# Optimization experiments

Measured on AMD Instinct MI355X. Metric: run time of the kernel, lower is better.

The kernel has to match this reference:

```python
import jax, jax.numpy as jnp
import numpy as np
import math

B, S, D, NH = 2, 2048, 1024, 16
DK = D // NH
E, TOPK, MOE_H, NSH = 8, 2, 1024, 2
SH_H = MOE_H * NSH
EPS = 1e-6


def setup_inputs() -> dict:
    key = jax.random.key(0)
    ks = jax.random.split(key, 24)
    p = lambda k, shape: jax.random.normal(k, shape, jnp.float32) * 0.02
    x = jax.random.normal(ks[0], (B, S, D), jnp.float32)
    # RoPE tables: freqs_cis = exp(i * t * theta^{-2j/dk}), passed as cos/sin
    inv = 1.0 / (10000.0 ** (np.arange(0, DK, 2, dtype=np.float32) / DK))
    ang = np.outer(np.arange(S, dtype=np.float32), inv)
    freqs_cos = jnp.asarray(np.cos(ang), jnp.float32)
    freqs_sin = jnp.asarray(np.sin(ang), jnp.float32)
    mask = jnp.triu(jnp.full((S, S), -1e9, jnp.float32), k=1)  # causal additive mask
    return {
        'x': x, 'freqs_cos': freqs_cos, 'freqs_sin': freqs_sin, 'mask': mask,
        'wq': p(ks[1], (D, D)), 'wk': p(ks[2], (D, D)),
        'wv': p(ks[3], (D, D)), 'wo': p(ks[4], (D, D)),
        'attn_norm_w': jnp.ones((D,), jnp.float32),
        'ffn_norm_w': jnp.ones((D,), jnp.float32),
        'gate_w': p(ks[5], (E, D)), 'gate_b': p(ks[6], (E,)),
        'w1': p(ks[7], (E, MOE_H, D)), 'b1': p(ks[8], (E, MOE_H)),
        'w2': p(ks[9], (E, D, MOE_H)), 'b2': p(ks[10], (E, D)),
        'w3': p(ks[11], (E, MOE_H, D)), 'b3': p(ks[12], (E, MOE_H)),
        'sg_w': p(ks[13], (SH_H, D)), 'su_w': p(ks[14], (SH_H, D)),
        'sd_w': p(ks[15], (D, SH_H)),
    }


def rmsnorm(x, w):
    f = x.astype(jnp.float32)
    y = f * jax.lax.rsqrt(jnp.mean(f * f, axis=-1, keepdims=True) + EPS)
    return y.astype(x.dtype) * w


def rope(t, cos, sin):
    # t: [b, s, h, dk]; pairs (t[2j], t[2j+1]) as complex, multiplied by e^{i ang}
    tr, ti = t[..., 0::2], t[..., 1::2]
    c, s = cos[None, :, None, :], sin[None, :, None, :]
    outr = tr * c - ti * s
    outi = tr * s + ti * c
    return jnp.stack([outr, outi], axis=-1).reshape(t.shape)


def reference(x, freqs_cos, freqs_sin, mask, wq, wk, wv, wo, attn_norm_w, ffn_norm_w,
              gate_w, gate_b, w1, b1, w2, b2, w3, b3, sg_w, su_w, sd_w):
    b, s, d = x.shape
    # --- attention with RoPE ---
    h = rmsnorm(x, attn_norm_w)
    q = (h @ wq.T).reshape(b, s, NH, DK)
    k = (h @ wk.T).reshape(b, s, NH, DK)
    v = (h @ wv.T).reshape(b, s, NH, DK)
    q = rope(q, freqs_cos, freqs_sin)
    k = rope(k, freqs_cos, freqs_sin)
    scale = 1.0 / math.sqrt(DK)
    q = q.transpose(0, 2, 1, 3)
    k = k.transpose(0, 2, 1, 3)
    v = v.transpose(0, 2, 1, 3)
    scores = jnp.einsum('bhqd,bhkd->bhqk', q, k) * scale + mask
    # NOTE: source divides by sqrt(d_k) a second time before softmax (faithful quirk)
    attn = jax.nn.softmax(scores * scale, axis=-1)
    o = jnp.einsum('bhqk,bhkd->bhqd', attn, v).transpose(0, 2, 1, 3).reshape(b, s, d)
    x = x + o @ wo.T
    # --- MoE FFN ---
    hf = rmsnorm(x, ffn_norm_w).reshape(-1, d)                 # [T, D]
    gscores = jax.nn.softmax(hf @ gate_w.T + gate_b, axis=-1)  # [T, E]
    _, idx = jax.lax.top_k(gscores, TOPK)                      # bias is None -> topk on scores
    weights = jnp.take_along_axis(gscores, idx, axis=1)        # original_scores gather
    wmask = (jax.nn.one_hot(idx, E, dtype=hf.dtype) * weights[..., None]).sum(1)  # [T, E]
    shared = (jax.nn.silu(hf @ sg_w.T) * (hf @ su_w.T)) @ sd_w.T
    a1 = jnp.einsum('td,ehd->teh', hf, w1) + b1
    a3 = jnp.einsum('td,ehd->teh', hf, w3) + b3
    eo = jnp.einsum('teh,edh->ted', jax.nn.silu(a1) * a3, w2) + b2  # [T, E, D]
    router = jnp.einsum('te,ted->td', wmask, eo)
    return x + (shared + router).reshape(x.shape)
```

## Files before the change

kernel.cpp:

```cpp
#include <hip/hip_runtime.h>


typedef unsigned short u16;
typedef __attribute__((ext_vector_type(8))) short bh8;
typedef __attribute__((ext_vector_type(4))) float fv4;
typedef __attribute__((ext_vector_type(4))) unsigned uv4;
typedef __attribute__((ext_vector_type(2))) int iv2;

#define LOG2E 1.4426950408889634f
#define MAX_TILES 71

__device__ __forceinline__ float b2f(u16 u) {
  return __builtin_bit_cast(float, ((unsigned)u) << 16);
}
__device__ __forceinline__ u16 f2b(float f) {
  unsigned x = __builtin_bit_cast(unsigned, f);
  return (u16)((x + 0x7fffu + ((x >> 16) & 1u)) >> 16);
}
__device__ __forceinline__ fv4 mfma16(bh8 a, bh8 b, fv4 c) {
  return __builtin_amdgcn_mfma_f32_16x16x32_bf16(a, b, c, 0, 0, 0);
}
__device__ __forceinline__ unsigned cvtpk(float lo, float hi) {
  unsigned r;
  asm("v_cvt_pk_bf16_f32 %0, %1, %2" : "=v"(r) : "v"(lo), "v"(hi));
  return r;
}

__device__ __forceinline__ int xcd_swizzle1d(int flat, int nwg) {
  int q = nwg >> 3, r = nwg & 7;
  int xcd = flat & 7, idx = flat >> 3;
  return (xcd < r ? xcd * (q + 1) : r * (q + 1) + (xcd - r) * q) + idx;
}

#define GLD16(g, l)                                                        \
  __builtin_amdgcn_global_load_lds(                                        \
      (const __attribute__((address_space(1))) void*)(g),                  \
      (__attribute__((address_space(3))) void*)(l), 16, 0, 0)

__device__ __forceinline__ bh8 lds_frag(const u16* base, int row, int b8) {
  int off = row * 128 + ((b8 * 16) ^ ((row & 7) << 4));
  return *(const bh8*)((const char*)base + off);
}

template <int MODE, int TM>
__device__ __forceinline__ void gemm_body(
    u16* AsB, u16* BsB, int bx, int by, const u16* __restrict__ A,
    const u16* __restrict__ B, int M, int N, int K, u16* __restrict__ Cb,
    float* __restrict__ Cf, const float* __restrict__ add1,
    const float* __restrict__ add2, const float* __restrict__ bias,
    const int* __restrict__ tmeta, const int* __restrict__ etok) {
  constexpr int MR = TM / 32;
  constexpr int ACL = TM / 64;
  const int lane = threadIdx.x & 63;
  const int wid = threadIdx.x >> 6;
  const int wr = wid >> 2, wc = wid & 3;
  const int n0 = bx * 128;
  const int l15 = lane & 15;
  const int rr = lane >> 3;
  const int b8s = (lane & 7) ^ rr;
  const int ldA = (MODE == 6) ? M : K;

  int m0 = 0, e = 0, m0l = 0, cnt = 0, row0 = 0;
  const u16* Bp = B;
  if constexpr (MODE == 6 || MODE == 8) {
    int tile = by, half = 0;
    if constexpr (MODE == 6 && TM == 64) {
      tile = by >> 1;
      half = by & 1;
    }
    if (tile >= tmeta[0]) return;
    e = tmeta[16 + tile * 4];
    m0l = tmeta[17 + tile * 4];
    cnt = tmeta[18 + tile * 4];
    row0 = tmeta[19 + tile * 4] + half * 64;
    Bp = B + (size_t)e * N * K;
  } else {
    m0 = by * TM;
  }

  const u16* Arow[ACL];
  const u16* Brow[2];
#pragma unroll
  for (int i = 0; i < ACL; ++i) {
    int c = wid * ACL + i;
    int row = c * 8 + rr;
    if constexpr (MODE == 8) {
      int li = m0l + row;
      li = li < cnt ? li : cnt - 1;
      int tok = etok[e * 4096 + li];
      Arow[i] = A + (size_t)tok * ldA + b8s * 8;
    } else if constexpr (MODE == 6) {
      Arow[i] = A + (size_t)(row0 + row) * ldA + b8s * 8;
    } else {
      Arow[i] = A + (size_t)(m0 + row) * ldA + b8s * 8;
    }
  }
#pragma unroll
  for (int i = 0; i < 2; ++i)
    Brow[i] = Bp + (size_t)(n0 + (wid * 2 + i) * 8 + rr) * K + b8s * 8;

  fv4 acc[MR][2] = {};
  const int nt = K >> 6;

#pragma unroll
  for (int i = 0; i < ACL; ++i)
    GLD16(Arow[i], &AsB[(wid * ACL + i) * 512]);
#pragma unroll
  for (int i = 0; i < 2; ++i)
    GLD16(Brow[i], &BsB[(wid * 2 + i) * 512]);

  for (int t = 0; t < nt; ++t) {
    const int cur = t & 1;
    u16* Asc = AsB + cur * (TM * 64);
    u16* Bsc = BsB + cur * (128 * 64);
    if (t + 1 < nt) {
      const int k0 = (t + 1) * 64;
      u16* Asn = AsB + (cur ^ 1) * (TM * 64);
      u16* Bsn = BsB + (cur ^ 1) * (128 * 64);
#pragma unroll
      for (int i = 0; i < ACL; ++i)
        GLD16(Arow[i] + k0, &Asn[(wid * ACL + i) * 512]);
#pragma unroll
      for (int i = 0; i < 2; ++i)
        GLD16(Brow[i] + k0, &Bsn[(wid * 2 + i) * 512]);
      if constexpr (ACL == 2)
        asm volatile("s_waitcnt vmcnt(4)" ::: "memory");
      else
        asm volatile("s_waitcnt vmcnt(3)" ::: "memory");
    } else {
      asm volatile("s_waitcnt vmcnt(0)" ::: "memory");
    }
    __builtin_amdgcn_s_barrier();
    __builtin_amdgcn_sched_barrier(0);

#pragma unroll
    for (int ks = 0; ks < 2; ++ks) {
      int b8 = ks * 4 + (lane >> 4);
      bh8 af[MR], bf[2];
#pragma unroll
      for (int mi = 0; mi < MR; ++mi)
        af[mi] = lds_frag(Asc, wr * (16 * MR) + mi * 16 + l15, b8);
      if constexpr (MODE == 7 || MODE == 8) {
        int col0 = (wc >> 1) * 64 + (wc & 1) * 16;
        bf[0] = lds_frag(Bsc, col0 + l15, b8);
        bf[1] = lds_frag(Bsc, col0 + 32 + l15, b8);
      } else {
#pragma unroll
        for (int ni = 0; ni < 2; ++ni)
          bf[ni] = lds_frag(Bsc, wc * 32 + ni * 16 + l15, b8);
      }
      __builtin_amdgcn_s_setprio(1);
#pragma unroll
      for (int mi = 0; mi < MR; ++mi)
#pragma unroll
        for (int ni = 0; ni < 2; ++ni)
          acc[mi][ni] = mfma16(af[mi], bf[ni], acc[mi][ni]);
      __builtin_amdgcn_s_setprio(0);
    }
    __builtin_amdgcn_sched_barrier(0);
    __builtin_amdgcn_s_barrier();
    __builtin_amdgcn_sched_barrier(0);
  }

  const int rbase = (MODE == 6 || MODE == 8) ? row0 : m0;
  const int r0b = rbase + wr * (16 * MR) + (lane >> 4) * 4;

  if constexpr (MODE == 7 || MODE == 8) {
    const int OUTN = N >> 1;
    const int c = (n0 >> 1) + (wc >> 1) * 32 + (wc & 1) * 16 + l15;
    const float* bb1 = nullptr;
    const float* bb3 = nullptr;
    if constexpr (MODE == 8) {
      bb1 = add1 + (size_t)e * OUTN;
      bb3 = add2 + (size_t)e * OUTN;
    }
#pragma unroll
    for (int mi = 0; mi < MR; ++mi) {
#pragma unroll
      for (int r = 0; r < 4; ++r) {
        int row = r0b + mi * 16 + r;
        float xg = acc[mi][0][r];
        float yu = acc[mi][1][r];
        if constexpr (MODE == 8) {
          xg += bb1[c];
          yu += bb3[c];
        }
        float s = xg / (1.f + __expf(-xg));
        Cb[(size_t)row * OUTN + c] = f2b(s * yu);
      }
    }
  } else if constexpr (MODE == 9) {
    const int c0b = n0 + wc * 32 + l15;
#pragma unroll
    for (int mi = 0; mi < MR; ++mi) {
#pragma unroll
      for (int r = 0; r < 4; ++r) {
        int row = r0b + mi * 16 + r;
        int g0 = tmeta[2 * row], g1 = tmeta[2 * row + 1];
        float w0 = bias[2 * row], w1 = bias[2 * row + 1];
        const u16* e0p = Cb + (size_t)g0 * 1024;
        const u16* e1p = Cb + (size_t)g1 * 1024;
#pragma unroll
        for (int ni = 0; ni < 2; ++ni) {
          int c = c0b + ni * 16;
          size_t idx = (size_t)row * N + c;
          Cf[idx] = add1[idx] + acc[mi][ni][r] + w0 * b2f(e0p[c]) +
                    w1 * b2f(e1p[c]);
        }
      }
    }
  } else {
    const int c0b = n0 + wc * 32 + l15;
    const float* bb = nullptr;
    if constexpr (MODE == 6) bb = bias + (size_t)e * N;
#pragma unroll
    for (int mi = 0; mi < MR; ++mi) {
#pragma unroll
      for (int ni = 0; ni < 2; ++ni) {
        int c = c0b + ni * 16;
#pragma unroll
        for (int r = 0; r < 4; ++r) {
          int row = r0b + mi * 16 + r;
          size_t idx = (size_t)row * N + c;
          float v = acc[mi][ni][r];
          if constexpr (MODE == 0) Cb[idx] = f2b(v);
          else if constexpr (MODE == 1) Cf[idx] = add1[idx] + v;
          else Cb[idx] = f2b(v + bb[c]);
        }
      }
    }
  }
}

template <int MODE, int TM = 128, int STILE = 0>
__global__ __launch_bounds__(512) void gemm_bt(
    const u16* __restrict__ A, const u16* __restrict__ B, int M, int N, int K,
    u16* __restrict__ Cb, float* __restrict__ Cf,
    const float* __restrict__ add1, const float* __restrict__ add2,
    const float* __restrict__ bias, const int* __restrict__ tmeta,
    const int* __restrict__ etok) {
  __shared__ u16 As[2][TM * 64];
  __shared__ u16 Bs[2][128 * 64];
  const int gx = gridDim.x;
  int flat = (int)blockIdx.y * gx + (int)blockIdx.x;
  flat = xcd_swizzle1d(flat, gx * (int)gridDim.y);
  int bx, by;
  if constexpr (STILE) {
    int SX = gx >> 2;
    int sidx = flat >> 5, within = flat & 31;
    int sy = sidx / SX, sx = sidx - sy * SX;
    by = sy * 8 + (within >> 2);
    bx = sx * 4 + (within & 3);
  } else {
    by = flat / gx;
    bx = flat - by * gx;
  }
  gemm_body<MODE, TM>(&As[0][0], &Bs[0][0], bx, by, A, B, M, N, K, Cb, Cf,
                      add1, add2, bias, tmeta, etok);
}

__global__ __launch_bounds__(512) void gemm_sgu_w13(
    const u16* __restrict__ hf, const u16* __restrict__ sgu_w,
    u16* __restrict__ hs, const u16* __restrict__ w13_w,
    u16* __restrict__ a13, const float* __restrict__ b1,
    const float* __restrict__ b3, const int* __restrict__ meta,
    const int* __restrict__ etok) {
  __shared__ u16 As[2][128 * 64];
  __shared__ u16 Bs[2][128 * 64];
  const int nwg = 1024 + 16 * MAX_TILES;
  int flat = xcd_swizzle1d((int)blockIdx.x, nwg);
  if (flat < 1024) {
    int sidx = flat >> 5, within = flat & 31;
    int sy = sidx >> 3, sx = sidx & 7;
    int by = sy * 8 + (within >> 2);
    int bx = sx * 4 + (within & 3);
    gemm_body<7, 128>(&As[0][0], &Bs[0][0], bx, by, hf, sgu_w, 4096, 4096,
                      1024, hs, nullptr, nullptr, nullptr, nullptr, nullptr,
                      nullptr);
  } else {
    int idx = flat - 1024;
    int by = idx >> 4, bx = idx & 15;
    gemm_body<8, 128>(&As[0][0], &Bs[0][0], bx, by, hf, w13_w, 4096, 2048,
                      1024, a13, nullptr, b1, b3, nullptr, meta, etok);
  }
}

__device__ __forceinline__ void conv_plain(const float* src, u16* dst,
                                           int lb) {
  size_t i = ((size_t)lb * 256 + threadIdx.x) * 8;
  fv4 a = *(const fv4*)(src + i);
  fv4 b = *(const fv4*)(src + i + 4);
  bh8 o;
#pragma unroll
  for (int j = 0; j < 4; ++j) o[j] = (short)f2b(a[j]);
#pragma unroll
  for (int j = 0; j < 4; ++j) o[4 + j] = (short)f2b(b[j]);
  *(bh8*)(dst + i) = o;
}
__device__ __forceinline__ void conv_ilv(const float* src, u16* dst, int lb,
                                         int half, int seg_shift) {
  size_t i = ((size_t)lb * 256 + threadIdx.x) * 8;
  int r = (int)(i >> 10), col = (int)(i & 1023);
  int rl = r & ((1 << seg_shift) - 1), e = r >> seg_shift;
  int dstrow = (e << (seg_shift + 1)) + ((rl >> 5) << 6) + (rl & 31) +
               (half << 5);
  fv4 a = *(const fv4*)(src + i);
  fv4 b = *(const fv4*)(src + i + 4);
  bh8 o;
#pragma unroll
  for (int j = 0; j < 4; ++j) o[j] = (short)f2b(a[j]);
#pragma unroll
  for (int j = 0; j < 4; ++j) o[4 + j] = (short)f2b(b[j]);
  *(bh8*)(dst + (size_t)dstrow * 1024 + col) = o;
}

__global__ __launch_bounds__(256) void mega_prep(
    const float* __restrict__ wq, const float* __restrict__ wk,
    const float* __restrict__ wv, const float* __restrict__ wo,
    const float* __restrict__ sdw, const float* __restrict__ w2,
    const float* __restrict__ sgw, const float* __restrict__ suw,
    const float* __restrict__ w1, const float* __restrict__ w3,
    const float* __restrict__ x, const float* __restrict__ anw,
    u16* __restrict__ wqkv_b, u16* __restrict__ wo_b,
    u16* __restrict__ sdw_b, u16* __restrict__ w2_b,
    u16* __restrict__ sgu_b, u16* __restrict__ w13_b,
    u16* __restrict__ h_b) {
  __shared__ float red[4];
  const int bid = blockIdx.x;
  if (bid < 512) {
    conv_plain(wq, wqkv_b, bid);
  } else if (bid < 1024) {
    conv_plain(wk, wqkv_b + 1048576, bid - 512);
  } else if (bid < 1536) {
    conv_plain(wv, wqkv_b + 2097152, bid - 1024);
  } else if (bid < 2048) {
    conv_plain(wo, wo_b, bid - 1536);
  } else if (bid < 3072) {
    conv_plain(sdw, sdw_b, bid - 2048);
  } else if (bid < 7168) {
    conv_plain(w2, w2_b, bid - 3072);
  } else if (bid < 8192) {
    conv_ilv(sgw, sgu_b, bid - 7168, 0, 11);
  } else if (bid < 9216) {
    conv_ilv(suw, sgu_b, bid - 8192, 1, 11);
  } else if (bid < 13312) {
    conv_ilv(w1, w13_b, bid - 9216, 0, 10);
  } else if (bid < 17408) {
    conv_ilv(w3, w13_b, bid - 13312, 1, 10);
  } else {
    int t = bid - 17408;
    const float* xr = x + (size_t)t * 1024;
    fv4 v = *(const fv4*)(xr + threadIdx.x * 4);
    float ss = v[0] * v[0] + v[1] * v[1] + v[2] * v[2] + v[3] * v[3];
#pragma unroll
    for (int off = 1; off < 64; off <<= 1) ss += __shfl_xor(ss, off);
    int lane = threadIdx.x & 63, wid = threadIdx.x >> 6;
    if (lane == 0) red[wid] = ss;
    __syncthreads();
    float inv =
        rsqrtf((red[0] + red[1] + red[2] + red[3]) * (1.0f / 1024.f) + 1e-6f);
    u16* op = h_b + (size_t)t * 1024 + threadIdx.x * 4;
    const float* wp = anw + threadIdx.x * 4;
#pragma unroll
    for (int i = 0; i < 4; ++i) op[i] = f2b(v[i] * inv * wp[i]);
  }
}

__global__ __launch_bounds__(256) void rope_repack(
    const u16* __restrict__ qkv, const float* __restrict__ fc,
    const float* __restrict__ fs, u16* __restrict__ qr, u16* __restrict__ kr,
    u16* __restrict__ vt, int S) {
  __shared__ u16 tile[64][65];
  const int s0 = blockIdx.x * 64;
  const int b = blockIdx.y;
  const int h0 = blockIdx.z * 4;
#pragma unroll 4
  for (int it = 0; it < 32; ++it) {
    int idx = threadIdx.x + it * 256;
    int tl = idx >> 7, rem = idx & 127;
    int h = h0 + (rem >> 5), i = rem & 31;
    int s = s0 + tl;
    float c = fc[s * 32 + i], sn = fs[s * 32 + i];
    size_t src = ((size_t)(b * S + s)) * 3072 + h * 64 + 2 * i;
    size_t dst = ((size_t)((b * 16 + h) * S + s)) * 64 + 2 * i;
    float a0 = b2f(qkv[src]), a1 = b2f(qkv[src + 1]);
    qr[dst] = f2b(a0 * c - a1 * sn);
    qr[dst + 1] = f2b(a0 * sn + a1 * c);
    float b0 = b2f(qkv[src + 1024]), b1 = b2f(qkv[src + 1025]);
    kr[dst] = f2b(b0 * c - b1 * sn);
    kr[dst + 1] = f2b(b0 * sn + b1 * c);
  }
  for (int hh = 0; hh < 4; ++hh) {
    int h = h0 + hh;
    __syncthreads();
    for (int cc = threadIdx.x; cc < 512; cc += 256) {
      int tl = cc >> 3, d8 = cc & 7;
      bh8 val = *(const bh8*)(qkv + ((size_t)(b * S + s0 + tl)) * 3072 + 2048 +
                              h * 64 + d8 * 8);
#pragma unroll
      for (int j = 0; j < 8; ++j) tile[tl][d8 * 8 + j] = (u16)val[j];
    }
    __syncthreads();
    for (int cc = threadIdx.x; cc < 512; cc += 256) {
      int d = cc >> 3, pg = cc & 7;
      int sbase = 16 * (pg >> 2) + 4 * (pg & 3);
      bh8 o;
#pragma unroll
      for (int j = 0; j < 8; ++j)
        o[j] = (short)tile[sbase + (j & 3) + ((j >> 2) << 5)][d];
      *(bh8*)(vt + ((size_t)((b * 16 + h) * 64 + d)) * S + s0 + pg * 8) = o;
    }
  }
}

__global__ __launch_bounds__(256) void attn_fwd(
    const u16* __restrict__ qr, const u16* __restrict__ kr,
    const u16* __restrict__ vt, u16* __restrict__ ob, int S, int NHc) {
  __shared__ u16 Ks[2][2][64 * 64];
  __shared__ u16 Vs[2][2][64 * 64];
  const int lane = threadIdx.x & 63;
  const int wid = threadIdx.x >> 6;
  const int g = lane >> 4;
  const int l15 = lane & 15;
  const int bh = blockIdx.x;
  const int ia = blockIdx.y;
  const int nq = S / 64;
  const int qa0 = ia * 64;
  const int qb0 = (nq - 1 - ia) * 64;
  const int b = bh / NHc, h = bh % NHc;
  const u16* qbase = qr + (size_t)bh * S * 64;
  const u16* kb = kr + (size_t)bh * S * 64;
  const u16* vb = vt + (size_t)bh * 64 * S;
  const float SC = 0.015625f * LOG2E;
  const int rr = lane >> 3;
  const int b8s = (lane & 7) ^ rr;

  bh8 ONES;
#pragma unroll
  for (int j = 0; j < 8; ++j) ONES[j] = (short)0x3f80;

  bh8 qfA[2], qfB[2];
  {
    const u16* qp = qbase + (size_t)(qa0 + wid * 16 + l15) * 64 + g * 8;
    qfA[0] = *(const bh8*)qp;
    qfA[1] = *(const bh8*)(qp + 32);
    qp = qbase + (size_t)(qb0 + wid * 16 + l15) * 64 + g * 8;
    qfB[0] = *(const bh8*)qp;
    qfB[1] = *(const bh8*)(qp + 32);
  }
  fv4 oaccA[4] = {}, oaccB[4] = {};
  fv4 lA = {}, lB = {};
  float mA = -1e30f, mB = -1e30f;
  const int nktB = nq - ia;
  const int nrounds = (nktB + 1) >> 1;

  auto stage = [&](int buf, int j0, int nsub) {
    for (int s = 0; s < nsub; ++s) {
#pragma unroll
      for (int i = 0; i < 2; ++i) {
        int c = wid * 2 + i;
        int row = c * 8 + rr;
        GLD16(kb + (size_t)(j0 + s * 64 + row) * 64 + b8s * 8,
              &Ks[buf][s][c * 512]);
        GLD16(vb + (size_t)row * S + j0 + s * 64 + b8s * 8,
              &Vs[buf][s][c * 512]);
      }
    }
  };
  stage(0, 0, nktB > 1 ? 2 : 1);

  auto process = [&](const bh8 (&kf)[2][4], const bh8 (&vf)[2][4], int j0,
                     int q0x, bh8* qf, fv4* oacc, float& mrow, fv4& lrowC) {
    const int q_my = q0x + wid * 16 + l15;
    fv4 st[4] = {};
    __builtin_amdgcn_s_setprio(1);
#pragma unroll
    for (int ks = 0; ks < 2; ++ks)
#pragma unroll
      for (int jt = 0; jt < 4; ++jt)
        st[jt] = mfma16(kf[ks][jt], qf[ks], st[jt]);
    __builtin_amdgcn_s_setprio(0);

    float sr[4][4];
    float mloc = -1e30f;
    const int jb = j0 + 4 * g;
    if (j0 + 63 > q0x + wid * 16) {
#pragma unroll
      for (int jt = 0; jt < 4; ++jt)
#pragma unroll
        for (int r = 0; r < 4; ++r) {
          int j = jb + jt * 16 + r;
          float s = (j <= q_my) ? st[jt][r] : -1e30f;
          sr[jt][r] = s;
          mloc = fmaxf(mloc, s);
        }
    } else {
#pragma unroll
      for (int jt = 0; jt < 4; ++jt)
#pragma unroll
        for (int r = 0; r < 4; ++r) {
          sr[jt][r] = st[jt][r];
          mloc = fmaxf(mloc, st[jt][r]);
        }
    }
    mloc = fmaxf(mloc, __shfl_xor(mloc, 16));
    mloc = fmaxf(mloc, __shfl_xor(mloc, 32));
    mloc *= SC;
    bool defer = __all(mloc <= mrow + 8.f);
    if (!defer) {
      float mnew = fmaxf(mrow, mloc);
      float sfac = exp2f(mrow - mnew);
      mrow = mnew;
      float sfC[4];
#pragma unroll
      for (int r = 0; r < 4; ++r) sfC[r] = __shfl(sfac, g * 4 + r);
#pragma unroll
      for (int dt = 0; dt < 4; ++dt)
#pragma unroll
        for (int r = 0; r < 4; ++r) oacc[dt][r] *= sfC[r];
#pragma unroll
      for (int r = 0; r < 4; ++r) lrowC[r] *= sfC[r];
    }
    float p[4][4];
#pragma unroll
    for (int jt = 0; jt < 4; ++jt)
#pragma unroll
      for (int r = 0; r < 4; ++r)
        p[jt][r] = exp2f(fmaf(sr[jt][r], SC, -mrow));

    __builtin_amdgcn_s_setprio(1);
    fv4 racc = {};
#pragma unroll
    for (int ks = 0; ks < 2; ++ks) {
      uv4 w;
      w[0] = cvtpk(p[ks][0], p[ks][1]);
      w[1] = cvtpk(p[ks][2], p[ks][3]);
      w[2] = cvtpk(p[ks + 2][0], p[ks + 2][1]);
      w[3] = cvtpk(p[ks + 2][2], p[ks + 2][3]);
      bh8 pa = __builtin_bit_cast(bh8, w);
      racc = mfma16(pa, ONES, racc);
#pragma unroll
      for (int dt = 0; dt < 4; ++dt)
        oacc[dt] = mfma16(pa, vf[ks][dt], oacc[dt]);
    }
    __builtin_amdgcn_s_setprio(0);
#pragma unroll
    for (int r = 0; r < 4; ++r) lrowC[r] += racc[r];
  };

  for (int rd = 0; rd < nrounds; ++rd) {
    __syncthreads();
    int rem = nktB - (rd + 1) * 2;
    if (rem > 0) stage((rd + 1) & 1, (rd + 1) * 128, rem > 1 ? 2 : 1);
#pragma unroll
    for (int s = 0; s < 2; ++s) {
      int kt = rd * 2 + s;
      if (kt >= nktB) break;
      const int j0 = kt * 64;
      const u16* Kc = Ks[rd & 1][s];
      const u16* Vc = Vs[rd & 1][s];
      bh8 kf[2][4], vf[2][4];
#pragma unroll
      for (int ks = 0; ks < 2; ++ks) {
        int b8 = ks * 4 + g;
#pragma unroll
        for (int jt = 0; jt < 4; ++jt)
          kf[ks][jt] = lds_frag(Kc, jt * 16 + l15, b8);
#pragma unroll
        for (int dt = 0; dt < 4; ++dt)
          vf[ks][dt] = lds_frag(Vc, dt * 16 + l15, b8);
      }
      process(kf, vf, j0, qb0, qfB, oaccB, mB, lB);
      if (kt <= ia) process(kf, vf, j0, qa0, qfA, oaccA, mA, lA);
    }
  }

  auto wout = [&](fv4* oacc, fv4 lrowC, int q0x) {
#pragma unroll
    for (int dt = 0; dt < 4; ++dt)
#pragma unroll
      for (int r = 0; r < 4; ++r) {
        int row = q0x + wid * 16 + g * 4 + r;
        int col = dt * 16 + l15;
        ob[((size_t)b * S + row) * 1024 + h * 64 + col] =
            f2b(oacc[dt][r] / lrowC[r]);
      }
  };
  wout(oaccA, lA, qa0);
  wout(oaccB, lB, qb0);
}

__global__ __launch_bounds__(256) void gate_topk(
    const float* __restrict__ x2, const float* __restrict__ nw,
    const float* __restrict__ gw, const float* __restrict__ gb,
    int* __restrict__ topk_e, float* __restrict__ topk_w,
    u16* __restrict__ hf) {
  int t = blockIdx.x * 4 + (threadIdx.x >> 6);
  int lane = threadIdx.x & 63;
  const float* xr = x2 + (size_t)t * 1024;
  float hv[16];
  float ss = 0.f;
#pragma unroll
  for (int i = 0; i < 4; ++i) {
    fv4 v = *(const fv4*)(xr + lane * 16 + i * 4);
#pragma unroll
    for (int j = 0; j < 4; ++j) {
      hv[i * 4 + j] = v[j];
      ss += v[j] * v[j];
    }
  }
#pragma unroll
  for (int off = 1; off < 64; off <<= 1) ss += __shfl_xor(ss, off);
  float inv = rsqrtf(ss * (1.0f / 1024.f) + 1e-6f);
  const fv4* nwp = (const fv4*)(nw + lane * 16);
#pragma unroll
  for (int i = 0; i < 4; ++i) {
    fv4 wv = nwp[i];
#pragma unroll
    for (int j = 0; j < 4; ++j) hv[i * 4 + j] *= inv * wv[j];
  }
  {
    bh8 o0, o1;
#pragma unroll
    for (int j = 0; j < 8; ++j) {
      o0[j] = (short)f2b(hv[j]);
      o1[j] = (short)f2b(hv[8 + j]);
    }
    u16* hp = hf + (size_t)t * 1024 + lane * 16;
    *(bh8*)hp = o0;
    *(bh8*)(hp + 8) = o1;
  }
  float logit[8];
#pragma unroll
  for (int e = 0; e < 8; ++e) {
    const fv4* wp = (const fv4*)(gw + (size_t)e * 1024 + lane * 16);
    float s = 0.f;
#pragma unroll
    for (int i = 0; i < 4; ++i) {
      fv4 wv = wp[i];
#pragma unroll
      for (int j = 0; j < 4; ++j) s += hv[i * 4 + j] * wv[j];
    }
    logit[e] = s;
  }
#pragma unroll
  for (int off = 1; off < 64; off <<= 1)
#pragma unroll
    for (int e = 0; e < 8; ++e) logit[e] += __shfl_xor(logit[e], off);
  if (lane == 0) {
#pragma unroll
    for (int e = 0; e < 8; ++e) logit[e] += gb[e];
    float mx = logit[0];
#pragma unroll
    for (int e = 1; e < 8; ++e) mx = fmaxf(mx, logit[e]);
    float pe[8], se = 0.f;
#pragma unroll
    for (int e = 0; e < 8; ++e) { pe[e] = __expf(logit[e] - mx); se += pe[e]; }
    float rs = 1.f / se;
#pragma unroll
    for (int e = 0; e < 8; ++e) pe[e] *= rs;
    int i0 = 0;
    float b0 = pe[0];
#pragma unroll
    for (int e = 1; e < 8; ++e)
      if (pe[e] > b0) { b0 = pe[e]; i0 = e; }
    int i1 = -1;
    float b1v = -1.f;
#pragma unroll
    for (int e = 0; e < 8; ++e)
      if (e != i0 && pe[e] > b1v) { b1v = pe[e]; i1 = e; }
    topk_e[2 * t] = i0;
    topk_e[2 * t + 1] = i1;
    topk_w[2 * t] = b0;
    topk_w[2 * t + 1] = b1v;
  }
}

__global__ __launch_bounds__(512) void route_tokens(
    const int* __restrict__ topk_e, int* __restrict__ pos_of,
    int* __restrict__ etok, int* __restrict__ meta, int* __restrict__ rowid,
    int T2) {
  __shared__ int scnt[8], sbase[8];
  const int e = threadIdx.x >> 6;
  const int lane = threadIdx.x & 63;
  int base = 0;
  for (int i0 = 0; i0 < T2; i0 += 128) {
    iv2 te = *(const iv2*)(topk_e + i0 + lane * 2);
    unsigned long long m0 = __ballot(te[0] == e);
    unsigned long long m1 = __ballot(te[1] == e);
    unsigned long long lt = (1ull << lane) - 1;
    int pre = __popcll(m0 & lt) + __popcll(m1 & lt);
    if (te[0] == e) {
      int pos = base + pre;
      etok[e * 4096 + pos] = (i0 >> 1) + lane;
      pos_of[i0 + lane * 2] = pos;
      ++pre;
    }
    if (te[1] == e) {
      int pos = base + pre;
      etok[e * 4096 + pos] = (i0 >> 1) + lane;
      pos_of[i0 + lane * 2 + 1] = pos;
    }
    base += __popcll(m0) + __popcll(m1);
  }
  if (lane == 0) scnt[e] = base;
  __syncthreads();
  if (threadIdx.x == 0) {
    int tt = 0, rb = 0;
#pragma unroll
    for (int e2 = 0; e2 < 8; ++e2) {
      sbase[e2] = rb;
      int c = scnt[e2];
      int nt = (c + 127) >> 7;
      for (int i = 0; i < nt; ++i) {
        meta[16 + tt * 4] = e2;
        meta[17 + tt * 4] = i * 128;
        meta[18 + tt * 4] = c;
        meta[19 + tt * 4] = rb + i * 128;
        ++tt;
      }
      rb += nt * 128;
    }
    meta[0] = tt;
  }
  __syncthreads();
  for (int i = threadIdx.x; i < T2; i += 512)
    rowid[i] = sbase[topk_e[i]] + pos_of[i];
}

extern "C" void kernel_launch(void* const* d_in, const int* in_sizes, int n_in,
                              void* d_out, int out_size, void* d_ws,
                              size_t ws_size, hipStream_t stream) {
  (void)in_sizes; (void)n_in; (void)out_size; (void)ws_size;
  const int Sc = 2048, Dc = 1024, NHc = 16, Tc = 4096, SH = 2048;

  const float* x   = (const float*)d_in[0];
  const float* fc  = (const float*)d_in[1];
  const float* fs  = (const float*)d_in[2];
  const float* wq  = (const float*)d_in[4];
  const float* wk  = (const float*)d_in[5];
  const float* wv  = (const float*)d_in[6];
  const float* wo  = (const float*)d_in[7];
  const float* anw = (const float*)d_in[8];
  const float* fnw = (const float*)d_in[9];
  const float* gw  = (const float*)d_in[10];
  const float* gb  = (const float*)d_in[11];
  const float* w1  = (const float*)d_in[12];
  const float* b1  = (const float*)d_in[13];
  const float* w2  = (const float*)d_in[14];
  const float* b2  = (const float*)d_in[15];
  const float* w3  = (const float*)d_in[16];
  const float* b3  = (const float*)d_in[17];
  const float* sgw = (const float*)d_in[18];
  const float* suw = (const float*)d_in[19];
  const float* sdw = (const float*)d_in[20];
  float* out = (float*)d_out;

  char* base = (char*)d_ws;
  size_t off = 0;
  auto alloc = [&](size_t bytes) -> void* {
    void* p = base + off;
    off += (bytes + 255) & ~(size_t)255;
    return p;
  };
  u16* wqkv_b = (u16*)alloc(2ull * 3072 * 1024);
  u16* wo_b   = (u16*)alloc(2ull * 1024 * 1024);
  u16* sgu_b  = (u16*)alloc(2ull * 4096 * 1024);
  u16* sdw_b  = (u16*)alloc(2ull * 1024 * 2048);
  u16* w13_b  = (u16*)alloc(2ull * 8 * 2048 * 1024);
  u16* w2_b   = (u16*)alloc(2ull * 8 * 1024 * 1024);
  char* regA = (char*)alloc(2ull * Tc * 4096);
  char* regB = (char*)alloc(2ull * (size_t)MAX_TILES * 128 * 2048);
  float* x2  = (float*)alloc(4ull * Tc * Dc);
  u16* hs_b  = (u16*)alloc(2ull * Tc * SH);
  int* topk_e = (int*)alloc(2ull * Tc * 4);
  float* topk_w = (float*)alloc(2ull * Tc * 4);
  int* pos_of = (int*)alloc(2ull * Tc * 4);
  int* rowid = (int*)alloc(2ull * Tc * 4);
  int* etok = (int*)alloc(8ull * 4096 * 4);
  int* meta = (int*)alloc(512 * 4);

  u16* qkv_out = (u16*)regA;
  u16* eo_c    = (u16*)regA;
  u16* h_b  = (u16*)regB;
  u16* qr   = (u16*)regB;
  u16* kr   = (u16*)(regB + 2ull * Tc * Dc);
  u16* vt_  = (u16*)(regB + 4ull * Tc * Dc);
  u16* o_b  = (u16*)(regB + 6ull * Tc * Dc);
  u16* a13_c = (u16*)regB;
  u16* hf_b = wqkv_b;

  mega_prep<<<dim3(21504), 256, 0, stream>>>(
      wq, wk, wv, wo, sdw, w2, sgw, suw, w1, w3, x, anw, wqkv_b, wo_b, sdw_b,
      w2_b, sgu_b, w13_b, h_b);

  gemm_bt<0, 128, 1><<<dim3(3072 / 128, Tc / 128), 512, 0, stream>>>(
      h_b, wqkv_b, Tc, 3072, Dc, qkv_out, nullptr, nullptr, nullptr, nullptr,
      nullptr, nullptr);
  rope_repack<<<dim3(Sc / 64, 2, 4), 256, 0, stream>>>(qkv_out, fc, fs, qr, kr,
                                                       vt_, Sc);
  attn_fwd<<<dim3(2 * NHc, Sc / 128), 256, 0, stream>>>(qr, kr, vt_, o_b, Sc,
                                                        NHc);
  gemm_bt<1, 64, 1><<<dim3(Dc / 128, Tc / 64), 512, 0, stream>>>(
      o_b, wo_b, Tc, Dc, Dc, nullptr, x2, x, nullptr, nullptr, nullptr,
      nullptr);

  gate_topk<<<Tc / 4, 256, 0, stream>>>(x2, fnw, gw, gb, topk_e, topk_w,
                                        hf_b);
  route_tokens<<<1, 512, 0, stream>>>(topk_e, pos_of, etok, meta, rowid,
                                      2 * Tc);

  gemm_sgu_w13<<<dim3(1024 + 16 * MAX_TILES), 512, 0, stream>>>(
      hf_b, sgu_b, hs_b, w13_b, a13_c, b1, b3, meta, etok);

  gemm_bt<6, 64><<<dim3(Dc / 128, 2 * MAX_TILES), 512, 0, stream>>>(
      a13_c, w2_b, 1024, Dc, 1024, eo_c, nullptr, nullptr, nullptr,
      b2, meta, etok);

  gemm_bt<9, 64, 1><<<dim3(Dc / 128, Tc / 64), 512, 0, stream>>>(
      hs_b, sdw_b, Tc, Dc, SH, eo_c, out, x2, nullptr, topk_w, rowid,
      nullptr);
}
```

Measured before the change: 363.3 us.

## Fuse RoPE and Q/K head repack into QKV GEMM epilogue

The QKV GEMM epilogue now applies RoPE to Q and K columns, pairing even and odd columns with a lane shuffle, and writes them straight into head-major layout. V is written to a compact buffer that a slimmer kernel then transposes. This drops one full read and write of the Q/K activations and the separate RoPE pass. In exchange the epilogue does scattered 2-byte stores and extra cos/sin loads, and the buffer aliasing is rearranged (qr moved, o_b now overlays h_b), which needs to stay correct.

```diff
diff --git a/kernel.cpp b/kernel.cpp
--- a/kernel.cpp
+++ b/kernel.cpp
@@ -206,6 +206,35 @@
           size_t idx = (size_t)row * N + c;
           Cf[idx] = add1[idx] + acc[mi][ni][r] + w0 * b2f(e0p[c]) +
                     w1 * b2f(e1p[c]);
+        }
+      }
+    }
+  } else if constexpr (MODE == 10) {
+    const int c0b = n0 + wc * 32 + l15;
+    u16* vbuf = (u16*)bias;
+    u16* kr = (u16*)Cf;
+#pragma unroll
+    for (int mi = 0; mi < MR; ++mi) {
+#pragma unroll
+      for (int ni = 0; ni < 2; ++ni) {
+        int c = c0b + ni * 16;
+#pragma unroll
+        for (int r = 0; r < 4; ++r) {
+          int row = r0b + mi * 16 + r;
+          float x = acc[mi][ni][r];
+          float p = __shfl_xor(x, 1);
+          if (c < 2048) {
+            int cc = c & 1023;
+            int i = (cc & 63) >> 1;
+            int s = row & 2047, bb = row >> 11;
+            float co = add1[s * 32 + i], si = add2[s * 32 + i];
+            float o = fmaf(p, (c & 1) ? si : -si, x * co);
+            u16* dst = (c < 1024) ? Cb : kr;
+            dst[((size_t)((bb * 16 + (cc >> 6)) * 2048 + s)) * 64 +
+                (cc & 63)] = f2b(o);
+          } else {
+            vbuf[(size_t)row * 1024 + (c - 2048)] = f2b(x);
+          }
         }
       }
     }
@@ -366,36 +395,18 @@
   }
 }
 
-__global__ __launch_bounds__(256) void rope_repack(
-    const u16* __restrict__ qkv, const float* __restrict__ fc,
-    const float* __restrict__ fs, u16* __restrict__ qr, u16* __restrict__ kr,
-    u16* __restrict__ vt, int S) {
+__global__ __launch_bounds__(256) void rope_v(const u16* __restrict__ vbuf,
+                                              u16* __restrict__ vt, int S) {
   __shared__ u16 tile[64][65];
   const int s0 = blockIdx.x * 64;
   const int b = blockIdx.y;
   const int h0 = blockIdx.z * 4;
-#pragma unroll 4
-  for (int it = 0; it < 32; ++it) {
-    int idx = threadIdx.x + it * 256;
-    int tl = idx >> 7, rem = idx & 127;
-    int h = h0 + (rem >> 5), i = rem & 31;
-    int s = s0 + tl;
-    float c = fc[s * 32 + i], sn = fs[s * 32 + i];
-    size_t src = ((size_t)(b * S + s)) * 3072 + h * 64 + 2 * i;
-    size_t dst = ((size_t)((b * 16 + h) * S + s)) * 64 + 2 * i;
-    float a0 = b2f(qkv[src]), a1 = b2f(qkv[src + 1]);
-    qr[dst] = f2b(a0 * c - a1 * sn);
-    qr[dst + 1] = f2b(a0 * sn + a1 * c);
-    float b0 = b2f(qkv[src + 1024]), b1 = b2f(qkv[src + 1025]);
-    kr[dst] = f2b(b0 * c - b1 * sn);
-    kr[dst + 1] = f2b(b0 * sn + b1 * c);
-  }
   for (int hh = 0; hh < 4; ++hh) {
     int h = h0 + hh;
     __syncthreads();
     for (int cc = threadIdx.x; cc < 512; cc += 256) {
       int tl = cc >> 3, d8 = cc & 7;
-      bh8 val = *(const bh8*)(qkv + ((size_t)(b * S + s0 + tl)) * 3072 + 2048 +
+      bh8 val = *(const bh8*)(vbuf + ((size_t)(b * S + s0 + tl)) * 1024 +
                               h * 64 + d8 * 8);
 #pragma unroll
       for (int j = 0; j < 8; ++j) tile[tl][d8 * 8 + j] = (u16)val[j];
@@ -780,13 +791,13 @@
   int* etok = (int*)alloc(8ull * 4096 * 4);
   int* meta = (int*)alloc(512 * 4);
 
-  u16* qkv_out = (u16*)regA;
-  u16* eo_c    = (u16*)regA;
+  u16* vbuf = (u16*)regA;
+  u16* eo_c = (u16*)regA;
   u16* h_b  = (u16*)regB;
-  u16* qr   = (u16*)regB;
   u16* kr   = (u16*)(regB + 2ull * Tc * Dc);
   u16* vt_  = (u16*)(regB + 4ull * Tc * Dc);
-  u16* o_b  = (u16*)(regB + 6ull * Tc * Dc);
+  u16* qr   = (u16*)(regB + 6ull * Tc * Dc);
+  u16* o_b  = (u16*)regB;
   u16* a13_c = (u16*)regB;
   u16* hf_b = wqkv_b;
 
@@ -794,11 +805,10 @@
       wq, wk, wv, wo, sdw, w2, sgw, suw, w1, w3, x, anw, wqkv_b, wo_b, sdw_b,
       w2_b, sgu_b, w13_b, h_b);
 
-  gemm_bt<0, 128, 1><<<dim3(3072 / 128, Tc / 128), 512, 0, stream>>>(
-      h_b, wqkv_b, Tc, 3072, Dc, qkv_out, nullptr, nullptr, nullptr, nullptr,
-      nullptr, nullptr);
-  rope_repack<<<dim3(Sc / 64, 2, 4), 256, 0, stream>>>(qkv_out, fc, fs, qr, kr,
-                                                       vt_, Sc);
+  gemm_bt<10, 128, 1><<<dim3(3072 / 128, Tc / 128), 512, 0, stream>>>(
+      h_b, wqkv_b, Tc, 3072, Dc, qr, (float*)kr, fc, fs,
+      (const float*)vbuf, nullptr, nullptr);
+  rope_v<<<dim3(Sc / 64, 2, 4), 256, 0, stream>>>(vbuf, vt_, Sc);
   attn_fwd<<<dim3(2 * NHc, Sc / 128), 256, 0, stream>>>(qr, kr, vt_, o_b, Sc,
                                                         NHc);
   gemm_bt<1, 64, 1><<<dim3(Dc / 128, Tc / 64), 512, 0, stream>>>(
```

New measurement: 358.4 us. No clear change (-1.3%).
